# Kernel tuning notes

Hardware: AMD Instinct MI355X
Metric: run time of the kernel (lower is better)

Reference implementation:

```python
import jax, jax.numpy as jnp
import numpy as np

B, S, D_MODEL, HEADS, DK = 2, 2048, 1024, 16, 64


def setup_inputs() -> dict:
    key = jax.random.key(0)
    ks = jax.random.split(key, 7)
    scale = 0.02
    return {
        "query": jax.random.normal(ks[0], (B, S, D_MODEL), jnp.float32),
        "key": jax.random.normal(ks[1], (B, S, D_MODEL), jnp.float32),
        "value": jax.random.normal(ks[2], (B, S, D_MODEL), jnp.float32),
        "Wq": jax.random.normal(ks[3], (D_MODEL, HEADS * DK), jnp.float32) * scale,
        "bq": jax.random.normal(ks[4], (HEADS * DK,), jnp.float32) * scale,
        "Wo": jax.random.normal(ks[5], (HEADS * DK, D_MODEL), jnp.float32) * scale,
        "bo": jax.random.normal(ks[6], (D_MODEL,), jnp.float32) * scale,
    }


def reference(query, key, value, Wq, bq, Wo, bo):
    # NOTE: faithful to the original code, which (buggily) uses _W_q to
    # project query, key AND value, and scales by sqrt(seq_len), not sqrt(d_k).
    seq_len = key.shape[1]

    def split_heads(x):
        # [B,S,H*DK] -> [H,B,S,DK]; torch chunk(dim=-1)+cat(dim=0) stacks head h
        # (slice h*DK:(h+1)*DK) at batch block h.
        p = x @ Wq + bq
        b, s, _ = p.shape
        return p.reshape(b, s, HEADS, DK).transpose(2, 0, 1, 3)

    q = split_heads(query)   # [H,B,S,DK]
    k = split_heads(key)
    v = split_heads(value)

    inv_scale = jnp.float32(1.0 / np.sqrt(seq_len))
    scores = jnp.einsum("hbqd,hbkd->hbqk", q, k) * inv_scale  # [H,B,S,S]
    attn = jax.nn.softmax(scores, axis=-1)
    out = jnp.einsum("hbqk,hbkd->hbqd", attn, v)  # [H,B,S,DK]
    # inverse of chunk(dim=0)+cat(dim=-1): [H,B,S,DK] -> [B,S,H*DK]
    out = out.transpose(1, 2, 0, 3).reshape(query.shape[0], query.shape[1], HEADS * DK)
    return out @ Wo + bo
```

## Files before the change

### kernel.cpp

```cpp
#include <hip/hip_runtime.h>

#define DEVI __device__ __forceinline__

typedef short short4_t __attribute__((ext_vector_type(4)));
typedef short short8_t __attribute__((ext_vector_type(8)));
typedef __bf16 bf16x8 __attribute__((ext_vector_type(8)));
typedef float f32x4 __attribute__((ext_vector_type(4)));

DEVI short f2bf(float f) {
    union { float f; unsigned u; } v; v.f = f;
    unsigned r = (v.u + 0x7fffu + ((v.u >> 16) & 1u)) >> 16;
    return (short)r;
}

DEVI unsigned pack_ru(float a, float b) {
    union { float f; unsigned u; } x, y; x.f = a; y.f = b;
    return __builtin_amdgcn_perm(y.u + 0x8000u, x.u + 0x8000u, 0x07060302u);
}

DEVI f32x4 pv_mfma(short4_t a, short4_t b, f32x4 c) {
#if defined(__HIP_DEVICE_COMPILE__)
#if __has_builtin(__builtin_amdgcn_mfma_f32_16x16x16bf16_1k)
    return __builtin_amdgcn_mfma_f32_16x16x16bf16_1k(a, b, c, 0, 0, 0);
#else
    union { short8_t s; bf16x8 b; } ua, ub;
    ua.s = (short8_t){a[0], a[1], a[2], a[3], 0, 0, 0, 0};
    ub.s = (short8_t){b[0], b[1], b[2], b[3], 0, 0, 0, 0};
    return __builtin_amdgcn_mfma_f32_16x16x32_bf16(ua.b, ub.b, c, 0, 0, 0);
#endif
#else
    (void)a; (void)b;
    return c;
#endif
}

DEVI void g2lds16(const short* g, short* l) {
    __builtin_amdgcn_global_load_lds(
        (const __attribute__((address_space(1))) void*)g,
        (__attribute__((address_space(3))) void*)l, 16, 0, 0);
}

__global__ __launch_bounds__(256) void cvt3_kernel(const float* __restrict__ q,
                                                   const float* __restrict__ k,
                                                   const float* __restrict__ v,
                                                   short* __restrict__ X) {
    const size_t N1 = (size_t)4096 * 1024;
    size_t e = ((size_t)blockIdx.x * 256 + threadIdx.x) * 4;
    const float* src; size_t off;
    if (e < N1)            { src = q; off = e; }
    else if (e < 2 * N1)   { src = k; off = e - N1; }
    else                   { src = v; off = e - 2 * N1; }
    f32x4 f = *(const f32x4*)(src + off);
    short4_t o;
    o[0] = f2bf(f[0]); o[1] = f2bf(f[1]); o[2] = f2bf(f[2]); o[3] = f2bf(f[3]);
    *(short4_t*)(X + e) = o;
}

__global__ __launch_bounds__(256) void transpose_w_kernel(const float* __restrict__ W,
                                                          short* __restrict__ Wt) {
    __shared__ short T[64][65];
    const int t = threadIdx.x;
    const int kt = blockIdx.x * 64, nt = blockIdx.y * 64;
#pragma unroll
    for (int r = 0; r < 4; ++r) {
        int kl = (t >> 4) + 16 * r;
        int n0 = (t & 15) * 4;
        f32x4 f = *(const f32x4*)(W + (size_t)(kt + kl) * 1024 + nt + n0);
#pragma unroll
        for (int j = 0; j < 4; ++j) T[n0 + j][kl] = f2bf(f[j]);
    }
    __syncthreads();
#pragma unroll
    for (int r = 0; r < 2; ++r) {
        int nl = (t >> 3) + 32 * r;
        int k0 = (t & 7) * 8;
        short8_t v;
#pragma unroll
        for (int j = 0; j < 8; ++j) v[j] = T[nl][k0 + j];
        *(short8_t*)(Wt + (size_t)(nt + nl) * 1024 + kt + k0) = v;
    }
}

template <typename OutT>
__global__ __launch_bounds__(256) void gemm_bt_kernel(const short* __restrict__ A,
                                                      const short* __restrict__ Bt,
                                                      const float* __restrict__ bias,
                                                      OutT* __restrict__ C,
                                                      int M, int N, int K,
                                                      int qrows, float qscale) {
    __shared__ __align__(16) short As[128 * 32];
    __shared__ __align__(16) short Bs[128 * 32];
    const int tid  = threadIdx.x;
    const int lane = tid & 63, wave = tid >> 6;
    const int quad = lane >> 4, l16 = lane & 15;
    const int row0 = blockIdx.x * 128, col0 = blockIdx.y * 128;
    const int wm = (wave >> 1) * 64, wn = (wave & 1) * 64;
    const int srow = lane >> 2;
    const int scol = (lane & 3) * 8;
    f32x4 acc[4][4] = {};
    for (int k0 = 0; k0 < K; k0 += 32) {
#pragma unroll
        for (int r = 0; r < 2; ++r) {
            int rb = r * 64 + wave * 16;
            g2lds16(A  + (size_t)(row0 + rb + srow) * K + k0 + scol, &As[rb * 32]);
            g2lds16(Bt + (size_t)(col0 + rb + srow) * K + k0 + scol, &Bs[rb * 32]);
        }
        __syncthreads();
        bf16x8 af[4], bfr[4];
#pragma unroll
        for (int mi = 0; mi < 4; ++mi) af[mi]  = *(const bf16x8*)&As[(wm + mi * 16 + l16) * 32 + quad * 8];
#pragma unroll
        for (int ni = 0; ni < 4; ++ni) bfr[ni] = *(const bf16x8*)&Bs[(wn + ni * 16 + l16) * 32 + quad * 8];
#pragma unroll
        for (int mi = 0; mi < 4; ++mi)
#pragma unroll
            for (int ni = 0; ni < 4; ++ni)
                acc[mi][ni] = __builtin_amdgcn_mfma_f32_16x16x32_bf16(af[mi], bfr[ni], acc[mi][ni], 0, 0, 0);
        __syncthreads();
    }
#pragma unroll
    for (int mi = 0; mi < 4; ++mi) {
#pragma unroll
        for (int ni = 0; ni < 4; ++ni) {
            int col = col0 + wn + ni * 16 + l16;
            float bv = bias[col];
#pragma unroll
            for (int i = 0; i < 4; ++i) {
                int row = row0 + wm + mi * 16 + quad * 4 + i;
                float val = acc[mi][ni][i] + bv;
                if (row < qrows) val *= qscale;
                if constexpr (sizeof(OutT) == 2) C[(size_t)row * N + col] = (OutT)f2bf(val);
                else                             C[(size_t)row * N + col] = (OutT)val;
            }
        }
    }
}

__global__ __launch_bounds__(256) void gemm_bt64_kernel(const short* __restrict__ A,
                                                        const short* __restrict__ Bt,
                                                        const float* __restrict__ bias,
                                                        float* __restrict__ C,
                                                        int M, int N, int K) {
    __shared__ __align__(16) short As[64 * 32];
    __shared__ __align__(16) short Bs[128 * 32];
    const int tid  = threadIdx.x;
    const int lane = tid & 63, wave = tid >> 6;
    const int quad = lane >> 4, l16 = lane & 15;
    const int row0 = blockIdx.x * 64, col0 = blockIdx.y * 128;
    const int wn = wave * 32;
    const int srow = lane >> 2;
    const int scol = (lane & 3) * 8;
    f32x4 acc[4][2] = {};
    for (int k0 = 0; k0 < K; k0 += 32) {
        {
            int rb = wave * 16;
            g2lds16(A + (size_t)(row0 + rb + srow) * K + k0 + scol, &As[rb * 32]);
        }
#pragma unroll
        for (int r = 0; r < 2; ++r) {
            int rb = r * 64 + wave * 16;
            g2lds16(Bt + (size_t)(col0 + rb + srow) * K + k0 + scol, &Bs[rb * 32]);
        }
        __syncthreads();
        bf16x8 af[4], bfr[2];
#pragma unroll
        for (int mi = 0; mi < 4; ++mi) af[mi]  = *(const bf16x8*)&As[(mi * 16 + l16) * 32 + quad * 8];
#pragma unroll
        for (int ni = 0; ni < 2; ++ni) bfr[ni] = *(const bf16x8*)&Bs[(wn + ni * 16 + l16) * 32 + quad * 8];
#pragma unroll
        for (int mi = 0; mi < 4; ++mi)
#pragma unroll
            for (int ni = 0; ni < 2; ++ni)
                acc[mi][ni] = __builtin_amdgcn_mfma_f32_16x16x32_bf16(af[mi], bfr[ni], acc[mi][ni], 0, 0, 0);
        __syncthreads();
    }
#pragma unroll
    for (int mi = 0; mi < 4; ++mi) {
#pragma unroll
        for (int ni = 0; ni < 2; ++ni) {
            int col = col0 + wn + ni * 16 + l16;
            float bv = bias[col];
#pragma unroll
            for (int i = 0; i < 4; ++i) {
                int row = row0 + mi * 16 + quad * 4 + i;
                C[(size_t)row * N + col] = acc[mi][ni][i] + bv;
            }
        }
    }
}

__global__ __launch_bounds__(256) void transpose_v_kernel(const short* __restrict__ Pv,
                                                          short* __restrict__ VT) {
    __shared__ short T[64][65];
    const int t = threadIdx.x;
    const int hb = blockIdx.x, st = blockIdx.y * 64;
    const int h = hb >> 1, b = hb & 1;
#pragma unroll
    for (int r = 0; r < 2; ++r) {
        int sl = (t >> 3) + 32 * r;
        short8_t v = *(const short8_t*)(Pv + (size_t)(b * 2048 + st + sl) * 1024 + h * 64 + (t & 7) * 8);
#pragma unroll
        for (int j = 0; j < 8; ++j) T[(t & 7) * 8 + j][sl] = v[j];
    }
    __syncthreads();
#pragma unroll
    for (int r = 0; r < 2; ++r) {
        int dl = (t >> 3) + 32 * r;
        short8_t v;
#pragma unroll
        for (int j = 0; j < 8; ++j) v[j] = T[dl][(t & 7) * 8 + j];
        *(short8_t*)(VT + ((size_t)hb * 64 + dl) * 2048 + st + (t & 7) * 8) = v;
    }
}

__global__ __launch_bounds__(512, 2) void attn_kernel(const short* __restrict__ P,
                                                      const short* __restrict__ VT,
                                                      short* __restrict__ O) {
    constexpr int LDK = 72;
    constexpr int LDV = 136;
    constexpr int LDO = 72;
    union SmemU {
        struct { short Ks[2][128 * LDK]; short Vs[2][64 * LDV]; } s;
        short OT[256 * LDO];
    };
    __shared__ __align__(16) SmemU sm;

    const int t = threadIdx.x;
    const int lane = t & 63, wave = t >> 6;
    const int quad = lane >> 4, l16 = lane & 15;
    const int bx = blockIdx.x;
    const int xcd = bx & 7, bi = bx >> 3;
    const int hb = xcd * 4 + (bi & 3), qt = bi >> 2;
    const int h = hb >> 1, b = hb & 1;
    const short* Pq  = P + (size_t)(b * 2048 + qt * 256) * 1024 + h * 64;
    const short* Pk  = P + (size_t)(4096 + b * 2048) * 1024 + h * 64;
    const short* VTh = VT + (size_t)hb * 64 * 2048;
    const int wq = wave * 32;

    bf16x8 qf[2][2];
#pragma unroll
    for (int miq = 0; miq < 2; ++miq)
#pragma unroll
        for (int kh = 0; kh < 2; ++kh)
            qf[miq][kh] = *(const bf16x8*)(Pq + (size_t)(wq + miq * 16 + l16) * 1024 + kh * 32 + quad * 8);

    float lrow[2] = {0.f, 0.f};
    f32x4 oacc[4][2] = {};

    const int krow = t >> 3, kc8 = (t & 7) * 8;
    const int vrow = t >> 4, vc8 = (t & 15) * 8;

    short8_t kreg[2], vreg[2];
#pragma unroll
    for (int it = 0; it < 2; ++it) {
        kreg[it] = *(const short8_t*)(Pk + (size_t)(it * 64 + krow) * 1024 + kc8);
        vreg[it] = *(const short8_t*)(VTh + (size_t)(it * 32 + vrow) * 2048 + vc8);
    }

    for (int tile = 0; tile < 16; ++tile) {
        const int buf = tile & 1;
        short* Ksb = sm.s.Ks[buf];
        short* Vsb = sm.s.Vs[buf];
#pragma unroll
        for (int it = 0; it < 2; ++it) {
            *(short8_t*)&Ksb[(it * 64 + krow) * LDK + kc8] = kreg[it];
            *(short8_t*)&Vsb[(it * 32 + vrow) * LDV + vc8] = vreg[it];
        }
        __syncthreads();
        if (tile + 1 < 16) {
            int kv0 = (tile + 1) * 128;
#pragma unroll
            for (int it = 0; it < 2; ++it) {
                kreg[it] = *(const short8_t*)(Pk + (size_t)(kv0 + it * 64 + krow) * 1024 + kc8);
                vreg[it] = *(const short8_t*)(VTh + (size_t)(it * 32 + vrow) * 2048 + kv0 + vc8);
            }
        }
#pragma unroll
        for (int kvc = 0; kvc < 8; ++kvc) {
            bf16x8 a0 = *(const bf16x8*)&Ksb[(kvc * 16 + l16) * LDK + quad * 8];
            bf16x8 a1 = *(const bf16x8*)&Ksb[(kvc * 16 + l16) * LDK + 32 + quad * 8];
            short4_t vA[4];
#pragma unroll
            for (int di = 0; di < 4; ++di)
                vA[di] = *(const short4_t*)&Vsb[(di * 16 + l16) * LDV + kvc * 16 + quad * 4];
#pragma unroll
            for (int miq = 0; miq < 2; ++miq) {
                f32x4 s = {};
                s = __builtin_amdgcn_mfma_f32_16x16x32_bf16(a0, qf[miq][0], s, 0, 0, 0);
                s = __builtin_amdgcn_mfma_f32_16x16x32_bf16(a1, qf[miq][1], s, 0, 0, 0);
                float p0 = __builtin_amdgcn_exp2f(s[0]);
                float p1 = __builtin_amdgcn_exp2f(s[1]);
                float p2 = __builtin_amdgcn_exp2f(s[2]);
                float p3 = __builtin_amdgcn_exp2f(s[3]);
                lrow[miq] += (p0 + p1) + (p2 + p3);
                union { uint2 u; short4_t s4; } pb;
                pb.u.x = pack_ru(p0, p1);
                pb.u.y = pack_ru(p2, p3);
#pragma unroll
                for (int di = 0; di < 4; ++di)
                    oacc[di][miq] = pv_mfma(vA[di], pb.s4, oacc[di][miq]);
            }
        }
        __syncthreads();
    }

    float rinv[2];
#pragma unroll
    for (int miq = 0; miq < 2; ++miq) {
        float ls = lrow[miq];
        ls += __shfl_xor(ls, 16);
        ls += __shfl_xor(ls, 32);
        rinv[miq] = 1.0f / ls;
    }

#pragma unroll
    for (int di = 0; di < 4; ++di) {
#pragma unroll
        for (int miq = 0; miq < 2; ++miq) {
            float v0 = oacc[di][miq][0] * rinv[miq];
            float v1 = oacc[di][miq][1] * rinv[miq];
            float v2 = oacc[di][miq][2] * rinv[miq];
            float v3 = oacc[di][miq][3] * rinv[miq];
            uint2 w;
            w.x = pack_ru(v0, v1);
            w.y = pack_ru(v2, v3);
            int q = wq + miq * 16 + l16;
            *(uint2*)&sm.OT[q * LDO + di * 16 + quad * 4] = w;
        }
    }
    __syncthreads();
    {
        const int orow = t >> 1, ocol = (t & 1) * 32;
        short* dst = O + (size_t)(b * 2048 + qt * 256 + orow) * 1024 + h * 64 + ocol;
#pragma unroll
        for (int c = 0; c < 4; ++c)
            *(short8_t*)(dst + c * 8) = *(const short8_t*)&sm.OT[orow * LDO + ocol + c * 8];
    }
}

extern "C" void kernel_launch(void* const* d_in, const int* in_sizes, int n_in,
                              void* d_out, int out_size, void* d_ws, size_t ws_size,
                              hipStream_t stream) {
    (void)in_sizes; (void)n_in; (void)out_size; (void)ws_size;
    const float* q  = (const float*)d_in[0];
    const float* k  = (const float*)d_in[1];
    const float* v  = (const float*)d_in[2];
    const float* Wq = (const float*)d_in[3];
    const float* bq = (const float*)d_in[4];
    const float* Wo = (const float*)d_in[5];
    const float* bo = (const float*)d_in[6];
    float* out = (float*)d_out;

    short* Xcat = (short*)d_ws;
    short* WqT  = Xcat + (size_t)12288 * 1024;
    short* WoT  = WqT + (size_t)1024 * 1024;
    short* P    = WoT + (size_t)1024 * 1024;
    short* VT   = P + (size_t)12288 * 1024;
    short* O    = VT + (size_t)32 * 64 * 2048;

    const float qscale = 0.022097086912079608f * 1.4426950408889634f;

    cvt3_kernel<<<12288, 256, 0, stream>>>(q, k, v, Xcat);
    transpose_w_kernel<<<dim3(16, 16), 256, 0, stream>>>(Wq, WqT);
    transpose_w_kernel<<<dim3(16, 16), 256, 0, stream>>>(Wo, WoT);
    gemm_bt_kernel<short><<<dim3(96, 8), 256, 0, stream>>>(Xcat, WqT, bq, P, 12288, 1024, 1024, 4096, qscale);
    transpose_v_kernel<<<dim3(32, 32), 256, 0, stream>>>(P + (size_t)8192 * 1024, VT);
    attn_kernel<<<256, 512, 0, stream>>>(P, VT, O);
    gemm_bt64_kernel<<<dim3(64, 8), 256, 0, stream>>>(O, WoT, bo, out, 4096, 1024, 1024);
}
```

Before: 219.8 us.

## Use 16x16x32 MFMA for PV and give each wave 64 query rows

The attention kernel moves from 8 waves of 32 query rows to 4 waves of 64 rows, halving block size so each K/V LDS fragment is reused across more queries. The PV product now uses the full-width 16x16x32 bf16 MFMA by pairing two 16-key score tiles into one 8-element P operand. K rows are permuted on the LDS store so the paired score tiles line up with the MFMA k-ordering. The cost is a doubled accumulator and Q-fragment register footprint per thread, which may lower occupancy or cause spills.

```diff
diff --git a/kernel.cpp b/kernel.cpp
--- a/kernel.cpp
+++ b/kernel.cpp
@@ -16,22 +16,6 @@
 DEVI unsigned pack_ru(float a, float b) {
     union { float f; unsigned u; } x, y; x.f = a; y.f = b;
     return __builtin_amdgcn_perm(y.u + 0x8000u, x.u + 0x8000u, 0x07060302u);
-}
-
-DEVI f32x4 pv_mfma(short4_t a, short4_t b, f32x4 c) {
-#if defined(__HIP_DEVICE_COMPILE__)
-#if __has_builtin(__builtin_amdgcn_mfma_f32_16x16x16bf16_1k)
-    return __builtin_amdgcn_mfma_f32_16x16x16bf16_1k(a, b, c, 0, 0, 0);
-#else
-    union { short8_t s; bf16x8 b; } ua, ub;
-    ua.s = (short8_t){a[0], a[1], a[2], a[3], 0, 0, 0, 0};
-    ub.s = (short8_t){b[0], b[1], b[2], b[3], 0, 0, 0, 0};
-    return __builtin_amdgcn_mfma_f32_16x16x32_bf16(ua.b, ub.b, c, 0, 0, 0);
-#endif
-#else
-    (void)a; (void)b;
-    return c;
-#endif
 }
 
 DEVI void g2lds16(const short* g, short* l) {
@@ -213,7 +197,7 @@
     }
 }
 
-__global__ __launch_bounds__(512, 2) void attn_kernel(const short* __restrict__ P,
+__global__ __launch_bounds__(256, 2) void attn_kernel(const short* __restrict__ P,
                                                       const short* __restrict__ VT,
                                                       short* __restrict__ O) {
     constexpr int LDK = 72;
@@ -235,26 +219,28 @@
     const short* Pq  = P + (size_t)(b * 2048 + qt * 256) * 1024 + h * 64;
     const short* Pk  = P + (size_t)(4096 + b * 2048) * 1024 + h * 64;
     const short* VTh = VT + (size_t)hb * 64 * 2048;
-    const int wq = wave * 32;
-
-    bf16x8 qf[2][2];
-#pragma unroll
-    for (int miq = 0; miq < 2; ++miq)
+    const int wq = wave * 64;
+
+    bf16x8 qf[4][2];
+#pragma unroll
+    for (int miq = 0; miq < 4; ++miq)
 #pragma unroll
         for (int kh = 0; kh < 2; ++kh)
             qf[miq][kh] = *(const bf16x8*)(Pq + (size_t)(wq + miq * 16 + l16) * 1024 + kh * 32 + quad * 8);
 
-    float lrow[2] = {0.f, 0.f};
-    f32x4 oacc[4][2] = {};
+    float lrow[4] = {0.f, 0.f, 0.f, 0.f};
+    f32x4 oacc[4][4] = {};
 
     const int krow = t >> 3, kc8 = (t & 7) * 8;
+    const int kj = krow & 7, kq = krow >> 3;
+    const int lrow32 = (kj >= 4 ? 16 + (kj - 4) : kj) + kq * 4;
     const int vrow = t >> 4, vc8 = (t & 15) * 8;
 
-    short8_t kreg[2], vreg[2];
-#pragma unroll
-    for (int it = 0; it < 2; ++it) {
-        kreg[it] = *(const short8_t*)(Pk + (size_t)(it * 64 + krow) * 1024 + kc8);
-        vreg[it] = *(const short8_t*)(VTh + (size_t)(it * 32 + vrow) * 2048 + vc8);
+    short8_t kreg[4], vreg[4];
+#pragma unroll
+    for (int it = 0; it < 4; ++it) {
+        kreg[it] = *(const short8_t*)(Pk + (size_t)(it * 32 + krow) * 1024 + kc8);
+        vreg[it] = *(const short8_t*)(VTh + (size_t)(it * 16 + vrow) * 2048 + vc8);
     }
 
     for (int tile = 0; tile < 16; ++tile) {
@@ -262,51 +248,61 @@
         short* Ksb = sm.s.Ks[buf];
         short* Vsb = sm.s.Vs[buf];
 #pragma unroll
-        for (int it = 0; it < 2; ++it) {
-            *(short8_t*)&Ksb[(it * 64 + krow) * LDK + kc8] = kreg[it];
-            *(short8_t*)&Vsb[(it * 32 + vrow) * LDV + vc8] = vreg[it];
+        for (int it = 0; it < 4; ++it) {
+            *(short8_t*)&Ksb[(it * 32 + lrow32) * LDK + kc8] = kreg[it];
+            *(short8_t*)&Vsb[(it * 16 + vrow) * LDV + vc8] = vreg[it];
         }
         __syncthreads();
         if (tile + 1 < 16) {
             int kv0 = (tile + 1) * 128;
 #pragma unroll
-            for (int it = 0; it < 2; ++it) {
-                kreg[it] = *(const short8_t*)(Pk + (size_t)(kv0 + it * 64 + krow) * 1024 + kc8);
-                vreg[it] = *(const short8_t*)(VTh + (size_t)(it * 32 + vrow) * 2048 + kv0 + vc8);
+            for (int it = 0; it < 4; ++it) {
+                kreg[it] = *(const short8_t*)(Pk + (size_t)(kv0 + it * 32 + krow) * 1024 + kc8);
+                vreg[it] = *(const short8_t*)(VTh + (size_t)(it * 16 + vrow) * 2048 + kv0 + vc8);
             }
         }
 #pragma unroll
-        for (int kvc = 0; kvc < 8; ++kvc) {
-            bf16x8 a0 = *(const bf16x8*)&Ksb[(kvc * 16 + l16) * LDK + quad * 8];
-            bf16x8 a1 = *(const bf16x8*)&Ksb[(kvc * 16 + l16) * LDK + 32 + quad * 8];
-            short4_t vA[4];
+        for (int p = 0; p < 4; ++p) {
+            bf16x8 aA0 = *(const bf16x8*)&Ksb[(p * 32 + l16) * LDK + quad * 8];
+            bf16x8 aA1 = *(const bf16x8*)&Ksb[(p * 32 + l16) * LDK + 32 + quad * 8];
+            bf16x8 aB0 = *(const bf16x8*)&Ksb[(p * 32 + 16 + l16) * LDK + quad * 8];
+            bf16x8 aB1 = *(const bf16x8*)&Ksb[(p * 32 + 16 + l16) * LDK + 32 + quad * 8];
+            bf16x8 vA[4];
 #pragma unroll
             for (int di = 0; di < 4; ++di)
-                vA[di] = *(const short4_t*)&Vsb[(di * 16 + l16) * LDV + kvc * 16 + quad * 4];
-#pragma unroll
-            for (int miq = 0; miq < 2; ++miq) {
-                f32x4 s = {};
-                s = __builtin_amdgcn_mfma_f32_16x16x32_bf16(a0, qf[miq][0], s, 0, 0, 0);
-                s = __builtin_amdgcn_mfma_f32_16x16x32_bf16(a1, qf[miq][1], s, 0, 0, 0);
-                float p0 = __builtin_amdgcn_exp2f(s[0]);
-                float p1 = __builtin_amdgcn_exp2f(s[1]);
-                float p2 = __builtin_amdgcn_exp2f(s[2]);
-                float p3 = __builtin_amdgcn_exp2f(s[3]);
-                lrow[miq] += (p0 + p1) + (p2 + p3);
-                union { uint2 u; short4_t s4; } pb;
-                pb.u.x = pack_ru(p0, p1);
-                pb.u.y = pack_ru(p2, p3);
+                vA[di] = *(const bf16x8*)&Vsb[(di * 16 + l16) * LDV + p * 32 + quad * 8];
+#pragma unroll
+            for (int miq = 0; miq < 4; ++miq) {
+                f32x4 sA = {}, sB = {};
+                sA = __builtin_amdgcn_mfma_f32_16x16x32_bf16(aA0, qf[miq][0], sA, 0, 0, 0);
+                sB = __builtin_amdgcn_mfma_f32_16x16x32_bf16(aB0, qf[miq][0], sB, 0, 0, 0);
+                sA = __builtin_amdgcn_mfma_f32_16x16x32_bf16(aA1, qf[miq][1], sA, 0, 0, 0);
+                sB = __builtin_amdgcn_mfma_f32_16x16x32_bf16(aB1, qf[miq][1], sB, 0, 0, 0);
+                float eA0 = __builtin_amdgcn_exp2f(sA[0]);
+                float eA1 = __builtin_amdgcn_exp2f(sA[1]);
+                float eA2 = __builtin_amdgcn_exp2f(sA[2]);
+                float eA3 = __builtin_amdgcn_exp2f(sA[3]);
+                float eB0 = __builtin_amdgcn_exp2f(sB[0]);
+                float eB1 = __builtin_amdgcn_exp2f(sB[1]);
+                float eB2 = __builtin_amdgcn_exp2f(sB[2]);
+                float eB3 = __builtin_amdgcn_exp2f(sB[3]);
+                lrow[miq] += ((eA0 + eA1) + (eA2 + eA3)) + ((eB0 + eB1) + (eB2 + eB3));
+                union { unsigned u[4]; bf16x8 b8; } pb;
+                pb.u[0] = pack_ru(eA0, eA1);
+                pb.u[1] = pack_ru(eA2, eA3);
+                pb.u[2] = pack_ru(eB0, eB1);
+                pb.u[3] = pack_ru(eB2, eB3);
 #pragma unroll
                 for (int di = 0; di < 4; ++di)
-                    oacc[di][miq] = pv_mfma(vA[di], pb.s4, oacc[di][miq]);
+                    oacc[di][miq] = __builtin_amdgcn_mfma_f32_16x16x32_bf16(vA[di], pb.b8, oacc[di][miq], 0, 0, 0);
             }
         }
         __syncthreads();
     }
 
-    float rinv[2];
-#pragma unroll
-    for (int miq = 0; miq < 2; ++miq) {
+    float rinv[4];
+#pragma unroll
+    for (int miq = 0; miq < 4; ++miq) {
         float ls = lrow[miq];
         ls += __shfl_xor(ls, 16);
         ls += __shfl_xor(ls, 32);
@@ -316,7 +312,7 @@
 #pragma unroll
     for (int di = 0; di < 4; ++di) {
 #pragma unroll
-        for (int miq = 0; miq < 2; ++miq) {
+        for (int miq = 0; miq < 4; ++miq) {
             float v0 = oacc[di][miq][0] * rinv[miq];
             float v1 = oacc[di][miq][1] * rinv[miq];
             float v2 = oacc[di][miq][2] * rinv[miq];
@@ -330,11 +326,10 @@
     }
     __syncthreads();
     {
-        const int orow = t >> 1, ocol = (t & 1) * 32;
-        short* dst = O + (size_t)(b * 2048 + qt * 256 + orow) * 1024 + h * 64 + ocol;
-#pragma unroll
-        for (int c = 0; c < 4; ++c)
-            *(short8_t*)(dst + c * 8) = *(const short8_t*)&sm.OT[orow * LDO + ocol + c * 8];
+        short* dst = O + (size_t)(b * 2048 + qt * 256 + t) * 1024 + h * 64;
+#pragma unroll
+        for (int c = 0; c < 8; ++c)
+            *(short8_t*)(dst + c * 8) = *(const short8_t*)&sm.OT[t * LDO + c * 8];
     }
 }
 
@@ -365,6 +360,6 @@
     transpose_w_kernel<<<dim3(16, 16), 256, 0, stream>>>(Wo, WoT);
     gemm_bt_kernel<short><<<dim3(96, 8), 256, 0, stream>>>(Xcat, WqT, bq, P, 12288, 1024, 1024, 4096, qscale);
     transpose_v_kernel<<<dim3(32, 32), 256, 0, stream>>>(P + (size_t)8192 * 1024, VT);
-    attn_kernel<<<256, 512, 0, stream>>>(P, VT, O);
+    attn_kernel<<<256, 256, 0, stream>>>(P, VT, O);
     gemm_bt64_kernel<<<dim3(64, 8), 256, 0, stream>>>(O, WoT, bo, out, 4096, 1024, 1024);
 }
```

Result: slower. 324.2 us (+47.5%).
